# Optimization experiments

Measured on AMD Instinct MI355X. Metric: run time of the kernel, lower is better.

## Reference

```python
import jax, jax.numpy as jnp
import numpy as np

EPS = 1e-15

def gmm_conv(x, src, dst, edge_attr, g, mu, sigma, root, bias, num_nodes):
    # PyG GMMConv: x_j -> Linear g (in -> K*out), Gaussian mixture weights from
    # pseudo-coords, mean aggregation over incoming edges, plus root linear + bias.
    E = edge_attr.shape[0]
    K, D = mu.shape
    out_ch = g.shape[1] // K
    xj = x[src] @ g                                   # [E, K*out]
    diff = edge_attr[:, None, :] - mu[None, :, :]     # [E, K, D]
    gauss = jnp.exp(-0.5 * jnp.sum(diff * diff / (EPS + sigma[None] ** 2), axis=-1))  # [E, K]
    msg = jnp.sum(xj.reshape(E, K, out_ch) * gauss[:, :, None], axis=1)  # [E, out]
    agg = jax.ops.segment_sum(msg, dst, num_segments=num_nodes)          # [N, out]
    cnt = jax.ops.segment_sum(jnp.ones((E,), x.dtype), dst, num_segments=num_nodes)
    agg = agg / jnp.maximum(cnt, 1.0)[:, None]        # mean aggregation
    return agg + x @ root + bias


def _make_params(key, sizes, kernel=3, dim=3):
    ps = {}
    for li, (cin, cout) in enumerate(sizes, start=1):
        k1, k2, k3, k4, key = jax.random.split(key, 5)
        ps[f"g{li}"] = jax.random.normal(k1, (cin, cout * kernel), jnp.float32) / np.sqrt(cin)
        ps[f"mu{li}"] = jax.random.normal(k2, (kernel, dim), jnp.float32)
        ps[f"sigma{li}"] = jnp.abs(jax.random.normal(k3, (kernel, dim), jnp.float32)) + 0.5
        ps[f"root{li}"] = jax.random.normal(k4, (cin, cout), jnp.float32) / np.sqrt(cin)
        ps[f"b{li}"] = jnp.zeros((cout,), jnp.float32)
    return ps


def setup_inputs() -> dict:
    key = jax.random.key(0)
    N, E = 100000, 3200000
    k1, k2, k3, k4 = jax.random.split(key, 4)
    inp = {
        "x": jax.random.normal(k1, (N, 3), jnp.float32),
        "edge_index": jax.random.randint(k2, (2, E), 0, N, jnp.int64),
        "edge_attr": jax.random.uniform(k3, (E, 3), jnp.float32),
    }
    inp.update(_make_params(k4, [(3, 8), (8, 16), (16, 8), (8, 4)]))
    return inp


def reference(x, edge_index, edge_attr,
              g1, mu1, sigma1, root1, b1,
              g2, mu2, sigma2, root2, b2,
              g3, mu3, sigma3, root3, b3,
              g4, mu4, sigma4, root4, b4):
    N = x.shape[0]
    src, dst = edge_index[0], edge_index[1]
    h = jax.nn.elu(gmm_conv(x, src, dst, edge_attr, g1, mu1, sigma1, root1, b1, N))
    h = jax.nn.elu(gmm_conv(h, src, dst, edge_attr, g2, mu2, sigma2, root2, b2, N))
    h = jax.nn.elu(gmm_conv(h, src, dst, edge_attr, g3, mu3, sigma3, root3, b3, N))
    h = gmm_conv(h, src, dst, edge_attr, g4, mu4, sigma4, root4, b4, N)
    return h
```

## Files before the change

### kernel.cpp

```cpp
#include <hip/hip_runtime.h>
#include <hip/hip_fp16.h>
#include <math.h>

#define TPB 256
#define BIG 1024
#define G_CHUNKS 512
#define NBCAP 1024
#define SCAP 7168


__global__ void histA_kernel(const int* __restrict__ dst, int* __restrict__ hist,
                             int E, int CE, int NB) {
    __shared__ int lh[NBCAP];
    int g = blockIdx.x, t = threadIdx.x;
    for (int b = t; b < NBCAP; b += BIG) lh[b] = 0;
    __syncthreads();
    int e0 = g * CE, e1 = min(e0 + CE, E);
    for (int e = e0 + t; e < e1; e += BIG) atomicAdd(&lh[dst[e] >> 7], 1);
    __syncthreads();
    for (int b = t; b < NB; b += BIG) hist[b * G_CHUNKS + g] = lh[b];
}

__global__ void base2_kernel(int* __restrict__ hist, int* __restrict__ bintotal) {
    __shared__ int buf[G_CHUNKS];
    int b = blockIdx.x, t = threadIdx.x;
    int v = hist[b * G_CHUNKS + t];
    buf[t] = v;
    __syncthreads();
    for (int off = 1; off < G_CHUNKS; off <<= 1) {
        int u = (t >= off) ? buf[t - off] : 0;
        __syncthreads();
        buf[t] += u;
        __syncthreads();
    }
    hist[b * G_CHUNKS + t] = buf[t] - v;
    if (t == G_CHUNKS - 1) bintotal[b] = buf[t];
}

__global__ void scanB_kernel(const int* __restrict__ bintotal, int* __restrict__ binstart,
                             int NB) {
    __shared__ int buf[1024];
    int t = threadIdx.x;
    int v = (t < NB) ? ((bintotal[t] + 7) & ~7) : 0;
    buf[t] = v;
    __syncthreads();
    for (int off = 1; off < 1024; off <<= 1) {
        int u = (t >= off) ? buf[t - off] : 0;
        __syncthreads();
        buf[t] += u;
        __syncthreads();
    }
    if (t < NB) binstart[t] = buf[t] - v;
    if (t == 1023) binstart[NB] = buf[1023];
}

__global__ void scatterC_kernel(const int* __restrict__ src, const int* __restrict__ dst,
                                const float* __restrict__ ea, const int* __restrict__ hist,
                                const int* __restrict__ binstart,
                                int2* __restrict__ tmp, int E, int CE, int NB) {
    __shared__ int lcur[NBCAP];
    int g = blockIdx.x, t = threadIdx.x;
    for (int b = t; b < NB; b += BIG) lcur[b] = binstart[b] + hist[b * G_CHUNKS + g];
    __syncthreads();
    int e0 = g * CE, e1 = min(e0 + CE, E);
    for (int e = e0 + t; e < e1; e += BIG) {
        int d = dst[e];
        int pos = atomicAdd(&lcur[d >> 7], 1);
        unsigned q0 = min((unsigned)(ea[(size_t)e * 3 + 0] * 16384.0f), 16383u);
        unsigned q1 = min((unsigned)(ea[(size_t)e * 3 + 1] * 16384.0f), 16383u);
        unsigned q2 = min((unsigned)(ea[(size_t)e * 3 + 2] * 4096.0f), 4095u);
        int2 rec;
        rec.x = (int)(q0 | (q1 << 14) | ((q2 & 0xFu) << 28));
        rec.y = (int)((unsigned)src[e] | ((unsigned)(d & 127) << 17) | ((q2 >> 4) << 24));
        tmp[pos] = rec;
    }
}

__global__ void binsortD_kernel(const int2* __restrict__ tmp,
                                const int* __restrict__ binstart,
                                const int* __restrict__ bintotal,
                                int2* __restrict__ perm,
                                int* __restrict__ rowstart, int* __restrict__ rowend,
                                int N, int NB) {
    __shared__ int2 stage[SCAP];
    __shared__ int h128[128], lcur[128];
    int b = blockIdx.x, t = threadIdx.x;
    int lo = binstart[b];
    int cnt = bintotal[b];
    int hi = lo + cnt;
    if (t < 128) h128[t] = 0;
    __syncthreads();
    for (int i = lo + t; i < hi; i += TPB) {
        unsigned y = (unsigned)tmp[i].y;
        atomicAdd(&h128[(y >> 17) & 127u], 1);
    }
    __syncthreads();
    if (t == 0) {
        int run = 0;
        for (int r = 0; r < 128; ++r) { int c = h128[r]; lcur[r] = run; run += c; }
    }
    __syncthreads();
    int n0 = b << 7;
    if (t < 128 && n0 + t < N) {
        rowstart[n0 + t] = lo + lcur[t];
        rowend[n0 + t]   = lo + lcur[t] + h128[t];
    }
    __syncthreads();
    if (cnt <= SCAP) {
        for (int i = lo + t; i < hi; i += TPB) {
            int2 v = tmp[i];
            int pos = atomicAdd(&lcur[((unsigned)v.y >> 17) & 127u], 1);
            stage[pos] = v;
        }
        __syncthreads();
        for (int j = t; j < cnt; j += TPB) perm[lo + j] = stage[j];
    } else {
        for (int i = lo + t; i < hi; i += TPB) {
            int2 v = tmp[i];
            int pos = atomicAdd(&lcur[((unsigned)v.y >> 17) & 127u], 1);
            perm[lo + pos] = v;
        }
    }
}

template<int CIN>
__device__ __forceinline__ void load_row(const float* p, float* hv) {
    if constexpr (CIN == 3) { hv[0] = p[0]; hv[1] = p[1]; hv[2] = p[2]; }
    else {
#pragma unroll
        for (int q = 0; q < CIN / 4; ++q) {
            float4 v = ((const float4*)p)[q];
            hv[4 * q + 0] = v.x; hv[4 * q + 1] = v.y;
            hv[4 * q + 2] = v.z; hv[4 * q + 3] = v.w;
        }
    }
}
template<int CIN>
__device__ __forceinline__ void load_row(const __half* p, float* hv) {
    if constexpr (CIN == 3) {
        hv[0] = __half2float(p[0]); hv[1] = __half2float(p[1]); hv[2] = __half2float(p[2]);
    } else {
#pragma unroll
        for (int q = 0; q < CIN / 8; ++q) {
            float4 v = ((const float4*)p)[q];
            const __half2* hp = (const __half2*)&v;
#pragma unroll
            for (int j = 0; j < 4; ++j) {
                float2 f = __half22float2(hp[j]);
                hv[8 * q + 2 * j + 0] = f.x;
                hv[8 * q + 2 * j + 1] = f.y;
            }
        }
    }
}
__device__ __forceinline__ void store_out(float* p, float v)  { *p = v; }
__device__ __forceinline__ void store_out(__half* p, float v) { *p = __float2half(v); }

template<typename TIN, typename TOUT, int CIN, int COUT, bool ELU, int LPN>
__global__ void layer_kernel(const TIN* __restrict__ h,
                             const float* __restrict__ g,
                             const float* __restrict__ mu, const float* __restrict__ sigma,
                             const float* __restrict__ root,
                             const float* __restrict__ bias,
                             const int* __restrict__ rowstart,
                             const int* __restrict__ rowend,
                             const int2* __restrict__ perm,
                             TOUT* __restrict__ out, int N) {
    __shared__ float s_g[CIN * 3 * COUT];
    __shared__ float s_root[CIN * COUT];
    __shared__ float s_b[COUT];
    __shared__ float s_mu[9], s_gs[9];
    int t = threadIdx.x;
    for (int i = t; i < CIN * 3 * COUT; i += TPB) s_g[i] = g[i];
    for (int i = t; i < CIN * COUT; i += TPB) s_root[i] = root[i];
    if (t < COUT) s_b[t] = bias[t];
    if (t < 9) {
        s_mu[t] = mu[t];
        float sg = sigma[t];
        s_gs[t] = -0.5f / (1e-15f + sg * sg);
    }
    __syncthreads();

    int gid = blockIdx.x * TPB + t;
    int n = gid / LPN;
    int sub = gid & (LPN - 1);
    bool active = n < N;

    float T[CIN][3] = {};
    int e0 = 0, e1 = 0;
    if (active) { e0 = rowstart[n]; e1 = rowend[n]; }

    int e = e0 + sub;
    int2 pnf;
    if (e < e1) pnf = perm[e];
    while (e < e1) {
        int2 p = pnf;
        int en = e + LPN;
        if (en < e1) pnf = perm[en];
        unsigned xw = (unsigned)p.x, yw = (unsigned)p.y;
        float u0 = ((float)(xw & 16383u) + 0.5f) * 6.103515625e-05f;
        float u1 = ((float)((xw >> 14) & 16383u) + 0.5f) * 6.103515625e-05f;
        unsigned q2 = ((xw >> 28) & 0xFu) | (((yw >> 24) & 0xFFu) << 4);
        float u2 = ((float)q2 + 0.5f) * 2.44140625e-04f;
        unsigned s = yw & 0x1FFFFu;
        float w[3];
#pragma unroll
        for (int k = 0; k < 3; ++k) {
            float d0 = u0 - s_mu[3 * k + 0];
            float d1 = u1 - s_mu[3 * k + 1];
            float d2 = u2 - s_mu[3 * k + 2];
            w[k] = __expf(d0 * d0 * s_gs[3 * k + 0] +
                          d1 * d1 * s_gs[3 * k + 1] +
                          d2 * d2 * s_gs[3 * k + 2]);
        }
        float hv[CIN];
        load_row<CIN>(h + (size_t)s * CIN, hv);
#pragma unroll
        for (int i = 0; i < CIN; ++i) {
            T[i][0] = fmaf(hv[i], w[0], T[i][0]);
            T[i][1] = fmaf(hv[i], w[1], T[i][1]);
            T[i][2] = fmaf(hv[i], w[2], T[i][2]);
        }
        e = en;
    }

#pragma unroll
    for (int i = 0; i < CIN; ++i)
#pragma unroll
        for (int k = 0; k < 3; ++k) {
            float v = T[i][k];
#pragma unroll
            for (int off = 1; off < LPN; off <<= 1)
                v += __shfl_xor(v, off);
            T[i][k] = v;
        }

    if (active) {
        float invd = 1.0f / fmaxf((float)(e1 - e0), 1.0f);
        float hv2[CIN];
        load_row<CIN>(h + (size_t)n * CIN, hv2);
#pragma unroll
        for (int j = 0; j < (COUT + LPN - 1) / LPN; ++j) {
            int o = sub + LPN * j;
            if (o < COUT) {
                float acc = 0.f;
#pragma unroll
                for (int i = 0; i < CIN; ++i)
#pragma unroll
                    for (int k = 0; k < 3; ++k)
                        acc = fmaf(T[i][k], s_g[(i * 3 + k) * COUT + o], acc);
                acc = acc * invd + s_b[o];
#pragma unroll
                for (int i = 0; i < CIN; ++i)
                    acc = fmaf(hv2[i], s_root[i * COUT + o], acc);
                if (ELU && acc < 0.f) acc = __expf(acc) - 1.0f;
                store_out(out + (size_t)n * COUT + o, acc);
            }
        }
    }
}

template<typename TIN, typename TOUT, int CIN, int COUT, bool ELU>
static void launch_layer(const TIN* hin, const float* g, const float* mu,
                         const float* sigma, const float* root, const float* b,
                         const int* rowstart, const int* rowend, const int2* perm,
                         TOUT* hout, int N, hipStream_t stream) {
    constexpr int LPN = 8;
    int blocks = ((size_t)N * LPN + TPB - 1) / TPB;
    layer_kernel<TIN, TOUT, CIN, COUT, ELU, LPN><<<blocks, TPB, 0, stream>>>(
        hin, g, mu, sigma, root, b, rowstart, rowend, perm, hout, N);
}

extern "C" void kernel_launch(void* const* d_in, const int* in_sizes, int n_in,
                              void* d_out, int out_size, void* d_ws, size_t ws_size,
                              hipStream_t stream) {
    const float* x  = (const float*)d_in[0];
    const int*   ei = (const int*)d_in[1];
    const float* ea = (const float*)d_in[2];

    const int N = in_sizes[0] / 3;
    const int E = in_sizes[2] / 3;
    const int* src = ei;
    const int* dst = ei + E;

    const float* g1 = (const float*)d_in[3];  const float* mu1 = (const float*)d_in[4];
    const float* s1 = (const float*)d_in[5];  const float* r1  = (const float*)d_in[6];
    const float* b1 = (const float*)d_in[7];
    const float* g2 = (const float*)d_in[8];  const float* mu2 = (const float*)d_in[9];
    const float* s2 = (const float*)d_in[10]; const float* r2  = (const float*)d_in[11];
    const float* b2 = (const float*)d_in[12];
    const float* g3 = (const float*)d_in[13]; const float* mu3 = (const float*)d_in[14];
    const float* s3 = (const float*)d_in[15]; const float* r3  = (const float*)d_in[16];
    const float* b3 = (const float*)d_in[17];
    const float* g4 = (const float*)d_in[18]; const float* mu4 = (const float*)d_in[19];
    const float* s4 = (const float*)d_in[20]; const float* r4  = (const float*)d_in[21];
    const float* b4 = (const float*)d_in[22];

    const int NB = (N + 127) >> 7;
    const int CE = (E + G_CHUNKS - 1) / G_CHUNKS;
    const int EPAD = E + 8 * NB;

    char* w = (char*)d_ws;
    int* rowstart = (int*)w;
    int* rowend   = rowstart + N;
    int* binstart = rowend + N;
    int* bintotal = binstart + (NB + 1);
    size_t off = (((size_t)(2 * N + 2 * NB + 1)) * 4 + 63) & ~(size_t)63;
    int2* tmp  = (int2*)(w + off);
    int2* perm = tmp + EPAD;
    __half* hA = (__half*)(perm + EPAD);
    __half* hB = hA + (size_t)N * 16;
    int* hist = (int*)(hB + (size_t)N * 16);

    histA_kernel<<<G_CHUNKS, BIG, 0, stream>>>(dst, hist, E, CE, NB);
    base2_kernel<<<NB, G_CHUNKS, 0, stream>>>(hist, bintotal);
    scanB_kernel<<<1, 1024, 0, stream>>>(bintotal, binstart, NB);
    scatterC_kernel<<<G_CHUNKS, BIG, 0, stream>>>(src, dst, ea, hist, binstart, tmp, E, CE, NB);
    binsortD_kernel<<<NB, TPB, 0, stream>>>(tmp, binstart, bintotal, perm, rowstart, rowend, N, NB);

    float* out = (float*)d_out;

    launch_layer<float,  __half, 3,  8,  true >(x,  g1, mu1, s1, r1, b1, rowstart, rowend, perm, hA, N, stream);
    launch_layer<__half, __half, 8,  16, true >(hA, g2, mu2, s2, r2, b2, rowstart, rowend, perm, hB, N, stream);
    launch_layer<__half, __half, 16, 8,  true >(hB, g3, mu3, s3, r3, b3, rowstart, rowend, perm, hA, N, stream);
    launch_layer<__half, float,  8,  4,  false>(hA, g4, mu4, s4, r4, b4, rowstart, rowend, perm, out, N, stream);
}
```

Measured before the change: 196.5 us.

## Stage scatter records in LDS by bin before writing to global

The scatter kernel now recounts its chunk's edges per bin, runs a block-wide prefix scan, and places the packed edge records into shared memory sorted by bin. It then copies them out in order so that consecutive threads write contiguous runs in each bin's global slot, which replaces the random per-edge global writes. This costs an extra pass over dst, a 1024-step scan with syncs, a binary search per output record and about 66KB of LDS that limits occupancy. The old direct kernel is kept as a fallback for chunks larger than the staging buffer.

Measured after the change: 183.2 us. -6.8%, faster.

```diff
diff --git a/kernel.cpp b/kernel.cpp
--- a/kernel.cpp
+++ b/kernel.cpp
@@ -7,6 +7,7 @@
 #define G_CHUNKS 512
 #define NBCAP 1024
 #define SCAP 7168
+#define SCAP2 6272
 
 
 __global__ void histA_kernel(const int* __restrict__ dst, int* __restrict__ hist,
@@ -55,6 +56,63 @@
 }
 
 __global__ void scatterC_kernel(const int* __restrict__ src, const int* __restrict__ dst,
+                                const float* __restrict__ ea, const int* __restrict__ hist,
+                                const int* __restrict__ binstart,
+                                int2* __restrict__ tmp, int E, int CE, int NB) {
+    __shared__ int lbase[NBCAP];
+    __shared__ int laux[NBCAP];
+    __shared__ int2 stage[SCAP2];
+    int g = blockIdx.x, t = threadIdx.x;
+    int e0 = g * CE, e1 = min(e0 + CE, E);
+    int total = e1 - e0;
+
+    for (int b = t; b < NBCAP; b += BIG) lbase[b] = 0;
+    __syncthreads();
+    for (int e = e0 + t; e < e1; e += BIG) atomicAdd(&lbase[dst[e] >> 7], 1);
+    __syncthreads();
+
+    int c = lbase[t];
+    laux[t] = c;
+    __syncthreads();
+    for (int off = 1; off < NBCAP; off <<= 1) {
+        int u = (t >= off) ? laux[t - off] : 0;
+        __syncthreads();
+        laux[t] += u;
+        __syncthreads();
+    }
+    int excl = laux[t] - c;
+    __syncthreads();
+    lbase[t] = excl;
+    laux[t] = 0;
+    __syncthreads();
+
+    for (int e = e0 + t; e < e1; e += BIG) {
+        int d = dst[e];
+        int b = d >> 7;
+        int pos = lbase[b] + atomicAdd(&laux[b], 1);
+        unsigned q0 = min((unsigned)(ea[(size_t)e * 3 + 0] * 16384.0f), 16383u);
+        unsigned q1 = min((unsigned)(ea[(size_t)e * 3 + 1] * 16384.0f), 16383u);
+        unsigned q2 = min((unsigned)(ea[(size_t)e * 3 + 2] * 4096.0f), 4095u);
+        int2 rec;
+        rec.x = (int)(q0 | (q1 << 14) | ((q2 & 0xFu) << 28));
+        rec.y = (int)((unsigned)src[e] | ((unsigned)(d & 127) << 17) | ((q2 >> 4) << 24));
+        stage[pos] = rec;
+    }
+    __syncthreads();
+
+    for (int b = t; b < NB; b += BIG) laux[b] = binstart[b] + hist[b * G_CHUNKS + g];
+    __syncthreads();
+    for (int j = t; j < total; j += BIG) {
+        int loB = 0, hiB = NB;
+        while (hiB - loB > 1) {
+            int mid = (loB + hiB) >> 1;
+            if (lbase[mid] <= j) loB = mid; else hiB = mid;
+        }
+        tmp[laux[loB] + (j - lbase[loB])] = stage[j];
+    }
+}
+
+__global__ void scatterC_direct(const int* __restrict__ src, const int* __restrict__ dst,
                                 const float* __restrict__ ea, const int* __restrict__ hist,
                                 const int* __restrict__ binstart,
                                 int2* __restrict__ tmp, int E, int CE, int NB) {
@@ -315,7 +373,11 @@
     histA_kernel<<<G_CHUNKS, BIG, 0, stream>>>(dst, hist, E, CE, NB);
     base2_kernel<<<NB, G_CHUNKS, 0, stream>>>(hist, bintotal);
     scanB_kernel<<<1, 1024, 0, stream>>>(bintotal, binstart, NB);
-    scatterC_kernel<<<G_CHUNKS, BIG, 0, stream>>>(src, dst, ea, hist, binstart, tmp, E, CE, NB);
+    if (CE <= SCAP2) {
+        scatterC_kernel<<<G_CHUNKS, BIG, 0, stream>>>(src, dst, ea, hist, binstart, tmp, E, CE, NB);
+    } else {
+        scatterC_direct<<<G_CHUNKS, BIG, 0, stream>>>(src, dst, ea, hist, binstart, tmp, E, CE, NB);
+    }
     binsortD_kernel<<<NB, TPB, 0, stream>>>(tmp, binstart, bintotal, perm, rowstart, rowend, N, NB);
 
     float* out = (float*)d_out;
```
